# Performance work log

Measured on AMD Instinct MI355X. Metric: run time of the kernel, lower is better.

## Reference

```python
import jax, jax.numpy as jnp
import numpy as np

V, D, HID, HEADS = 50000, 128, 128, 4
N, E, G = 100000, 1600000, 256
CH = HID // HEADS  # per-head channels for layer 1


def setup_inputs() -> dict:
    key = jax.random.key(0)
    ks = jax.random.split(key, 16)
    g = lambda i, shape, scale=0.05: jax.random.normal(ks[i], shape, jnp.float32) * scale
    return {
        "x_lex": jax.random.randint(ks[0], (N,), 0, V),
        "edge_index": jax.random.randint(ks[1], (2, E), 0, N),
        "batch": jnp.sort(jax.random.randint(ks[2], (N,), 0, G)),
        "emb": g(3, (V, D)),
        "W1": g(4, (D, HID)), "a1_src": g(5, (HEADS, CH)), "a1_dst": g(6, (HEADS, CH)), "b1": jnp.zeros((HID,), jnp.float32),
        "W2": g(7, (HID, HID)), "a2_src": g(8, (1, HID)), "a2_dst": g(9, (1, HID)), "b2": jnp.zeros((HID,), jnp.float32),
        "Wc1": g(10, (HID, HID // 2)), "bc1": jnp.zeros((HID // 2,), jnp.float32),
        "Wc2": g(11, (HID // 2, 1)), "bc2": jnp.zeros((1,), jnp.float32),
    }


def gat_layer(x, src, dst, W, a_src, a_dst, b, heads, ch):
    """PyG-style GATConv (v1), concat=True, negative_slope=0.2."""
    n = x.shape[0]
    h = (x @ W).reshape(n, heads, ch)                 # [N,H,C]
    al_s = (h * a_src).sum(-1)                        # [N,H]
    al_d = (h * a_dst).sum(-1)                        # [N,H]
    e = jax.nn.leaky_relu(al_s[src] + al_d[dst], 0.2) # [Etot,H]
    # segment softmax over incoming edges per destination node
    m = jax.ops.segment_max(e, dst, num_segments=n)
    ex = jnp.exp(e - m[dst])
    s = jax.ops.segment_sum(ex, dst, num_segments=n)
    alpha = ex / s[dst]
    out = jax.ops.segment_sum(alpha[:, :, None] * h[src], dst, num_segments=n)  # [N,H,C]
    return out.reshape(n, heads * ch) + b


def reference(x_lex, edge_index, batch, emb, W1, a1_src, a1_dst, b1, W2, a2_src, a2_dst, b2, Wc1, bc1, Wc2, bc2):
    n = x_lex.shape[0]
    loops = jnp.arange(n)  # GATConv adds self-loops by default
    src = jnp.concatenate([edge_index[0], loops])
    dst = jnp.concatenate([edge_index[1], loops])
    x = emb[x_lex]                                               # [N,D]
    h = jax.nn.elu(gat_layer(x, src, dst, W1, a1_src, a1_dst, b1, HEADS, CH))
    h = jax.nn.elu(gat_layer(h, src, dst, W2, a2_src, a2_dst, b2, 1, HID))
    sums = jax.ops.segment_sum(h, batch, num_segments=G)
    cnt = jax.ops.segment_sum(jnp.ones((n,), h.dtype), batch, num_segments=G)
    h_pool = sums / jnp.maximum(cnt, 1.0)[:, None]               # global mean pool [G,HID]
    logits = jax.nn.relu(h_pool @ Wc1 + bc1) @ Wc2 + bc2         # [G,1]
    return (logits, h_pool)
```

## Files before the change

kernel.cpp:

```cpp
#include <hip/hip_runtime.h>
#include <hip/hip_bf16.h>
#include <math.h>

#define P_CHUNK 8192
#define NBKT 1024

__device__ __forceinline__ float lrelu(float x){ return x < 0.f ? 0.2f*x : x; }
__device__ __forceinline__ float elu_(float x){ return x > 0.f ? x : expm1f(x); }

__global__ __launch_bounds__(256) void p1hist(const int* __restrict__ ei, int E, int Etot,
                                              int* __restrict__ totals){
  __shared__ int lh[NBKT];
  int tid = threadIdx.x;
  for (int t = tid; t < NBKT; t += 256) lh[t] = 0;
  __syncthreads();
  int base = blockIdx.x * P_CHUNK;
  for (int j = 0; j < P_CHUNK; j += 256){
    int i = base + j + tid;
    if (i < Etot){
      int dst = (i < E) ? ei[E + i] : (i - E);
      atomicAdd(&lh[dst >> 7], 1);
    }
  }
  __syncthreads();
  for (int t = tid; t < NBKT; t += 256){
    int v = lh[t];
    if (v) atomicAdd(&totals[t], v);
  }
}

__global__ __launch_bounds__(256) void p2scan(const int* __restrict__ totals,
                                              int* __restrict__ bbase, int* __restrict__ bcur,
                                              int Etot, int* __restrict__ off, int N){
  __shared__ int wsum[4];
  __shared__ int runsh;
  int tid = threadIdx.x, lane = tid & 63, w = tid >> 6;
  if (tid == 0) runsh = 0;
  __syncthreads();
  for (int c = 0; c < NBKT; c += 256){
    int v = totals[c + tid];
    int x = v;
    #pragma unroll
    for (int d = 1; d < 64; d <<= 1){ int y = __shfl_up(x, d); if (lane >= d) x += y; }
    if (lane == 63) wsum[w] = x;
    __syncthreads();
    int wpre = 0;
    for (int i = 0; i < w; i++) wpre += wsum[i];
    int run = runsh;
    int excl = run + wpre + x - v;
    bbase[c + tid] = excl;
    bcur[c + tid]  = excl;
    __syncthreads();
    if (tid == 0) runsh = run + wsum[0] + wsum[1] + wsum[2] + wsum[3];
    __syncthreads();
  }
  if (tid == 0){ bbase[NBKT] = Etot; off[N] = Etot; }
}

__global__ __launch_bounds__(256) void p3scatter(const int* __restrict__ ei, int E, int Etot,
                                                 int* __restrict__ bcur, int2* __restrict__ tmp){
  __shared__ int lh[NBKT];
  __shared__ int lbase[NBKT];
  int tid = threadIdx.x;
  for (int t = tid; t < NBKT; t += 256) lh[t] = 0;
  __syncthreads();
  int base = blockIdx.x * P_CHUNK;
  for (int j = 0; j < P_CHUNK; j += 256){
    int i = base + j + tid;
    if (i < Etot){
      int dst = (i < E) ? ei[E + i] : (i - E);
      atomicAdd(&lh[dst >> 7], 1);
    }
  }
  __syncthreads();
  for (int t = tid; t < NBKT; t += 256){
    int v = lh[t];
    lbase[t] = v ? atomicAdd(&bcur[t], v) : 0;
  }
  __syncthreads();
  for (int t = tid; t < NBKT; t += 256) lh[t] = 0;
  __syncthreads();
  for (int j = 0; j < P_CHUNK; j += 256){
    int i = base + j + tid;
    if (i < Etot){
      int s, d;
      if (i < E){ s = ei[i]; d = ei[E + i]; } else { s = i - E; d = i - E; }
      int b = d >> 7;
      int r = atomicAdd(&lh[b], 1);
      tmp[lbase[b] + r] = make_int2(s, d);
    }
  }
}

__global__ __launch_bounds__(256) void p4local(const int2* __restrict__ tmp,
                                               const int* __restrict__ bbase,
                                               int* __restrict__ off, int* __restrict__ srcs, int N){
  __shared__ int cnt[128];
  __shared__ int offL[128];
  int b = blockIdx.x, tid = threadIdx.x;
  int e0 = bbase[b], e1 = bbase[b + 1];
  if (tid < 128) cnt[tid] = 0;
  __syncthreads();
  for (int j = e0 + tid; j < e1; j += 256)
    atomicAdd(&cnt[tmp[j].y & 127], 1);
  __syncthreads();
  if (tid < 64){
    int v0 = cnt[2*tid], v1 = cnt[2*tid + 1];
    int p = v0 + v1;
    int x = p;
    #pragma unroll
    for (int d = 1; d < 64; d <<= 1){ int y = __shfl_up(x, d); if (tid >= d) x += y; }
    int excl = x - p;
    offL[2*tid]     = excl;
    offL[2*tid + 1] = excl + v0;
  }
  __syncthreads();
  if (tid < 128){
    int gd = b*128 + tid;
    if (gd < N) off[gd] = e0 + offL[tid];
    cnt[tid] = 0;
  }
  __syncthreads();
  for (int j = e0 + tid; j < e1; j += 256){
    int2 e = tmp[j];
    int d = e.y & 127;
    int r = atomicAdd(&cnt[d], 1);
    srcs[e0 + offL[d] + r] = e.x;
  }
}

template<int H, bool GATHER>
__global__ __launch_bounds__(256) void gemm_al(
    const float* __restrict__ X, const int* __restrict__ idx,
    const float* __restrict__ W, const float* __restrict__ asrc,
    const float* __restrict__ adst, float* __restrict__ Hout,
    float* __restrict__ als, float* __restrict__ ald, int n)
{
  __shared__ float xs[128][68];
  __shared__ float wch[32][128];
  int tid = threadIdx.x;
  int tr = tid >> 5, tc = tid & 31;
  int r8 = tr*8, c4 = tc*4;
  int row0 = blockIdx.x * 64;

  #pragma unroll
  for (int j=0;j<8;j++){
    int e = tid + j*256;
    int r = e >> 5, cq = e & 31;
    int gr = row0 + r;
    float4 v = make_float4(0.f,0.f,0.f,0.f);
    if (gr < n){
      int srow = GATHER ? idx[gr] : gr;
      v = *reinterpret_cast<const float4*>(&X[(size_t)srow*128 + cq*4]);
    }
    xs[cq*4+0][r] = v.x;
    xs[cq*4+1][r] = v.y;
    xs[cq*4+2][r] = v.z;
    xs[cq*4+3][r] = v.w;
  }

  float acc[8][4];
  #pragma unroll
  for (int r=0;r<8;r++)
    #pragma unroll
    for (int i=0;i<4;i++) acc[r][i] = 0.f;

  for (int kc=0;kc<4;kc++){
    __syncthreads();
    #pragma unroll
    for (int j=0;j<4;j++){
      int e = tid + j*256;
      int r = e>>5, cq = e&31;
      *reinterpret_cast<float4*>(&wch[r][cq*4]) =
        *reinterpret_cast<const float4*>(&W[(size_t)(kc*32+r)*128 + cq*4]);
    }
    __syncthreads();
    #pragma unroll
    for (int kk=0;kk<32;kk++){
      int k = kc*32+kk;
      const float4 x0 = *reinterpret_cast<const float4*>(&xs[k][r8]);
      const float4 x1 = *reinterpret_cast<const float4*>(&xs[k][r8+4]);
      const float4 wv = *reinterpret_cast<const float4*>(&wch[kk][c4]);
      acc[0][0]=fmaf(x0.x,wv.x,acc[0][0]); acc[0][1]=fmaf(x0.x,wv.y,acc[0][1]);
      acc[0][2]=fmaf(x0.x,wv.z,acc[0][2]); acc[0][3]=fmaf(x0.x,wv.w,acc[0][3]);
      acc[1][0]=fmaf(x0.y,wv.x,acc[1][0]); acc[1][1]=fmaf(x0.y,wv.y,acc[1][1]);
      acc[1][2]=fmaf(x0.y,wv.z,acc[1][2]); acc[1][3]=fmaf(x0.y,wv.w,acc[1][3]);
      acc[2][0]=fmaf(x0.z,wv.x,acc[2][0]); acc[2][1]=fmaf(x0.z,wv.y,acc[2][1]);
      acc[2][2]=fmaf(x0.z,wv.z,acc[2][2]); acc[2][3]=fmaf(x0.z,wv.w,acc[2][3]);
      acc[3][0]=fmaf(x0.w,wv.x,acc[3][0]); acc[3][1]=fmaf(x0.w,wv.y,acc[3][1]);
      acc[3][2]=fmaf(x0.w,wv.z,acc[3][2]); acc[3][3]=fmaf(x0.w,wv.w,acc[3][3]);
      acc[4][0]=fmaf(x1.x,wv.x,acc[4][0]); acc[4][1]=fmaf(x1.x,wv.y,acc[4][1]);
      acc[4][2]=fmaf(x1.x,wv.z,acc[4][2]); acc[4][3]=fmaf(x1.x,wv.w,acc[4][3]);
      acc[5][0]=fmaf(x1.y,wv.x,acc[5][0]); acc[5][1]=fmaf(x1.y,wv.y,acc[5][1]);
      acc[5][2]=fmaf(x1.y,wv.z,acc[5][2]); acc[5][3]=fmaf(x1.y,wv.w,acc[5][3]);
      acc[6][0]=fmaf(x1.z,wv.x,acc[6][0]); acc[6][1]=fmaf(x1.z,wv.y,acc[6][1]);
      acc[6][2]=fmaf(x1.z,wv.z,acc[6][2]); acc[6][3]=fmaf(x1.z,wv.w,acc[6][3]);
      acc[7][0]=fmaf(x1.w,wv.x,acc[7][0]); acc[7][1]=fmaf(x1.w,wv.y,acc[7][1]);
      acc[7][2]=fmaf(x1.w,wv.z,acc[7][2]); acc[7][3]=fmaf(x1.w,wv.w,acc[7][3]);
    }
  }

  const float4 asv = *reinterpret_cast<const float4*>(&asrc[c4]);
  const float4 adv = *reinterpret_cast<const float4*>(&adst[c4]);
  const int GT = 32 / H;
  int hh = tc / GT;

  #pragma unroll
  for (int r=0;r<8;r++){
    int gr = row0 + r8 + r;
    if (gr < n){
      *reinterpret_cast<float4*>(&Hout[(size_t)gr*128 + c4]) =
        make_float4(acc[r][0], acc[r][1], acc[r][2], acc[r][3]);
    }
    float ps = acc[r][0]*asv.x + acc[r][1]*asv.y + acc[r][2]*asv.z + acc[r][3]*asv.w;
    float pd = acc[r][0]*adv.x + acc[r][1]*adv.y + acc[r][2]*adv.z + acc[r][3]*adv.w;
    #pragma unroll
    for (int m=1;m<GT;m<<=1){ ps += __shfl_xor(ps,m); pd += __shfl_xor(pd,m); }
    if ((tc & (GT-1)) == 0 && gr < n){
      als[(size_t)gr*H + hh] = ps;
      ald[(size_t)gr*H + hh] = pd;
    }
  }
}

template<int H>
__global__ __launch_bounds__(256) void aggr(
    const float* __restrict__ h, const float* __restrict__ als,
    const float* __restrict__ ald, const int* __restrict__ srcs,
    const int* __restrict__ off, const float* __restrict__ bias,
    float* __restrict__ out, int n)
{
  __shared__ float s_p[4][64*H];
  __shared__ int   s_s[4][64];
  int tid = threadIdx.x;
  int wid = tid >> 6, lane = tid & 63;
  int d = blockIdx.x*4 + wid;
  if (d >= n) return;
  int half = lane >> 5, ch = lane & 31;
  int c4 = ch*4;
  const int hh = (H==1) ? 0 : (ch >> 3);

  int s0 = off[d], s1 = off[d+1];

  float adv[H];
  #pragma unroll
  for (int q=0;q<H;q++) adv[q] = ald[(size_t)d*H + q];

  float m[H], ssum[H];
  #pragma unroll
  for (int q=0;q<H;q++){ m[q] = -INFINITY; ssum[q] = 0.f; }
  float a0=0.f, a1=0.f, a2=0.f, a3=0.f;

  for (int base = s0; base < s1; base += 64){
    int cl = s1 - base; if (cl > 64) cl = 64;

    int sv = 0;
    float e[H];
    if (lane < cl){
      sv = srcs[base + lane];
      #pragma unroll
      for (int q=0;q<H;q++) e[q] = lrelu(als[(size_t)sv*H + q] + adv[q]);
    } else {
      #pragma unroll
      for (int q=0;q<H;q++) e[q] = -INFINITY;
    }

    float cm[H];
    #pragma unroll
    for (int q=0;q<H;q++) cm[q] = e[q];
    #pragma unroll
    for (int sh=1; sh<64; sh<<=1){
      #pragma unroll
      for (int q=0;q<H;q++) cm[q] = fmaxf(cm[q], __shfl_xor(cm[q], sh));
    }

    float p[H], sc[H];
    #pragma unroll
    for (int q=0;q<H;q++){
      float nm = fmaxf(m[q], cm[q]);
      sc[q] = __expf(m[q] - nm);
      ssum[q] *= sc[q];
      m[q] = nm;
      p[q] = __expf(e[q] - nm);
    }
    float schh = sc[0];
    #pragma unroll
    for (int q=1;q<H;q++) schh = (hh==q) ? sc[q] : schh;
    a0 *= schh; a1 *= schh; a2 *= schh; a3 *= schh;

    float cs[H];
    #pragma unroll
    for (int q=0;q<H;q++) cs[q] = p[q];
    #pragma unroll
    for (int sh=1; sh<64; sh<<=1){
      #pragma unroll
      for (int q=0;q<H;q++) cs[q] += __shfl_xor(cs[q], sh);
    }
    #pragma unroll
    for (int q=0;q<H;q++) ssum[q] += cs[q];

    #pragma unroll
    for (int q=0;q<H;q++) s_p[wid][lane*H + q] = p[q];
    s_s[wid][lane] = sv;

    for (int j = half; j < cl; j += 2){
      int s = s_s[wid][j];
      float w = s_p[wid][j*H + hh];
      const float4 hv = *reinterpret_cast<const float4*>(&h[(size_t)s*128 + c4]);
      a0 = fmaf(w, hv.x, a0);
      a1 = fmaf(w, hv.y, a1);
      a2 = fmaf(w, hv.z, a2);
      a3 = fmaf(w, hv.w, a3);
    }
  }

  a0 += __shfl_xor(a0, 32);
  a1 += __shfl_xor(a1, 32);
  a2 += __shfl_xor(a2, 32);
  a3 += __shfl_xor(a3, 32);

  float den = ssum[0];
  #pragma unroll
  for (int q=1;q<H;q++) den = (hh==q) ? ssum[q] : den;
  float inv = 1.f / den;

  if (half == 0){
    const float4 bv = *reinterpret_cast<const float4*>(&bias[c4]);
    float4 o;
    o.x = elu_(a0*inv + bv.x);
    o.y = elu_(a1*inv + bv.y);
    o.z = elu_(a2*inv + bv.z);
    o.w = elu_(a3*inv + bv.w);
    *reinterpret_cast<float4*>(&out[(size_t)d*128 + c4]) = o;
  }
}

__global__ __launch_bounds__(256) void kpool(const float* __restrict__ act,
    const int* __restrict__ batch, int n, float* __restrict__ pool)
{
  __shared__ int sb[2];
  __shared__ float part[128];
  int g = blockIdx.x, tid = threadIdx.x;
  if (tid == 0){
    int lo=0, hi=n;
    while (lo<hi){ int mid=(lo+hi)>>1; if (batch[mid] < g) lo=mid+1; else hi=mid; }
    sb[0]=lo;
    int lo2=lo, hi2=n;
    while (lo2<hi2){ int mid=(lo2+hi2)>>1; if (batch[mid] < g+1) lo2=mid+1; else hi2=mid; }
    sb[1]=lo2;
  }
  __syncthreads();
  int lo=sb[0], hi=sb[1];
  int c = tid & 127, half = tid >> 7;
  float acc = 0.f;
  for (int i=lo+half; i<hi; i+=2) acc += act[(size_t)i*128 + c];
  if (half == 0) part[c] = acc;
  __syncthreads();
  if (half == 1) part[c] += acc;
  __syncthreads();
  if (half == 0){
    float cnt = (float)(hi-lo);
    pool[(size_t)g*128 + c] = part[c] / fmaxf(cnt, 1.f);
  }
}

__global__ __launch_bounds__(64) void kclassify(const float* __restrict__ pool,
    const float* __restrict__ Wc1, const float* __restrict__ bc1,
    const float* __restrict__ Wc2, const float* __restrict__ bc2,
    float* __restrict__ logits)
{
  int g = blockIdx.x, j = threadIdx.x;
  const float* hp = pool + (size_t)g*128;
  float t = bc1[j];
  #pragma unroll 8
  for (int c=0;c<128;c++) t = fmaf(hp[c], Wc1[c*64+j], t);
  t = fmaxf(t, 0.f) * Wc2[j];
  for (int m=1;m<64;m<<=1) t += __shfl_xor(t, m);
  if (j==0) logits[g] = t + bc2[0];
}

extern "C" void kernel_launch(void* const* d_in, const int* in_sizes, int n_in,
                              void* d_out, int out_size, void* d_ws, size_t ws_size,
                              hipStream_t stream)
{
  const int*   x_lex = (const int*)d_in[0];
  const int*   ei    = (const int*)d_in[1];
  const int*   batch = (const int*)d_in[2];
  const float* emb   = (const float*)d_in[3];
  const float* W1    = (const float*)d_in[4];
  const float* a1s   = (const float*)d_in[5];
  const float* a1d   = (const float*)d_in[6];
  const float* b1    = (const float*)d_in[7];
  const float* W2    = (const float*)d_in[8];
  const float* a2s   = (const float*)d_in[9];
  const float* a2d   = (const float*)d_in[10];
  const float* b2    = (const float*)d_in[11];
  const float* Wc1   = (const float*)d_in[12];
  const float* bc1   = (const float*)d_in[13];
  const float* Wc2   = (const float*)d_in[14];
  const float* bc2   = (const float*)d_in[15];

  int N = in_sizes[0];
  int E = in_sizes[1] / 2;
  int Etot = E + N;
  const int G = 256;

  char* p = (char*)d_ws;
  float* hbuf   = (float*)p;          p += (size_t)N*128*4;
  float* act    = (float*)p;          p += (size_t)N*128*4;
  float* als    = (float*)p;          p += (size_t)N*4*4;
  float* ald    = (float*)p;          p += (size_t)N*4*4;
  int*   off    = (int*)p;            p += (size_t)(N+1)*4;
  int*   srcs   = (int*)p;            p += (size_t)Etot*4;
  int*   totals = (int*)p;            p += NBKT*4;
  int*   bbase  = (int*)p;            p += (NBKT+1)*4;
  int*   bcur   = (int*)p;
  int2*  tmp    = (int2*)hbuf;

  hipMemsetAsync(totals, 0, NBKT*4, stream);
  int nblk = (Etot + P_CHUNK - 1) / P_CHUNK;
  int nb   = (N + 127) / 128;
  p1hist   <<<nblk,256,0,stream>>>(ei, E, Etot, totals);
  p2scan   <<<1,   256,0,stream>>>(totals, bbase, bcur, Etot, off, N);
  p3scatter<<<nblk,256,0,stream>>>(ei, E, Etot, bcur, tmp);
  p4local  <<<nb,  256,0,stream>>>(tmp, bbase, off, srcs, N);

  int gb = (N + 63)/64;
  gemm_al<4,true ><<<gb,256,0,stream>>>(emb, x_lex, W1, a1s, a1d, hbuf, als, ald, N);
  aggr<4><<<(N+3)/4,256,0,stream>>>(hbuf, als, ald, srcs, off, b1, act, N);

  gemm_al<1,false><<<gb,256,0,stream>>>(act, nullptr, W2, a2s, a2d, hbuf, als, ald, N);
  aggr<1><<<(N+3)/4,256,0,stream>>>(hbuf, als, ald, srcs, off, b2, act, N);

  float* out = (float*)d_out;
  kpool<<<G,256,0,stream>>>(act, batch, N, out + G);
  kclassify<<<G,64,0,stream>>>(out + G, Wc1, bc1, Wc2, bc2, out);
}
```

Baseline: 528.3 us.

## Pack edge temp to 32-bit, row-major GEMM tile, nontemporal aggr stores

Packs the temporary (src, local dst) edge pair into a single 32-bit int (17 bits of source, 7 bits of local destination), halving the scatter and local-sort traffic. Changes the GEMM shared X tile from transposed to row-major with vector stores and a k-by-4 inner loop, removing the scalar transposing stores. Uses nontemporal stores for the aggregation output. The packing assumes N fits in 17 bits and is wrong for larger graphs.

```diff
diff --git a/kernel.cpp b/kernel.cpp
--- a/kernel.cpp
+++ b/kernel.cpp
@@ -4,6 +4,8 @@
 
 #define P_CHUNK 8192
 #define NBKT 1024
+
+typedef float f4 __attribute__((ext_vector_type(4)));
 
 __device__ __forceinline__ float lrelu(float x){ return x < 0.f ? 0.2f*x : x; }
 __device__ __forceinline__ float elu_(float x){ return x > 0.f ? x : expm1f(x); }
@@ -58,7 +60,7 @@
 }
 
 __global__ __launch_bounds__(256) void p3scatter(const int* __restrict__ ei, int E, int Etot,
-                                                 int* __restrict__ bcur, int2* __restrict__ tmp){
+                                                 int* __restrict__ bcur, int* __restrict__ tmp){
   __shared__ int lh[NBKT];
   __shared__ int lbase[NBKT];
   int tid = threadIdx.x;
@@ -87,12 +89,12 @@
       if (i < E){ s = ei[i]; d = ei[E + i]; } else { s = i - E; d = i - E; }
       int b = d >> 7;
       int r = atomicAdd(&lh[b], 1);
-      tmp[lbase[b] + r] = make_int2(s, d);
-    }
-  }
-}
-
-__global__ __launch_bounds__(256) void p4local(const int2* __restrict__ tmp,
+      tmp[lbase[b] + r] = s | ((d & 127) << 17);
+    }
+  }
+}
+
+__global__ __launch_bounds__(256) void p4local(const int* __restrict__ tmp,
                                                const int* __restrict__ bbase,
                                                int* __restrict__ off, int* __restrict__ srcs, int N){
   __shared__ int cnt[128];
@@ -102,7 +104,7 @@
   if (tid < 128) cnt[tid] = 0;
   __syncthreads();
   for (int j = e0 + tid; j < e1; j += 256)
-    atomicAdd(&cnt[tmp[j].y & 127], 1);
+    atomicAdd(&cnt[(tmp[j] >> 17) & 127], 1);
   __syncthreads();
   if (tid < 64){
     int v0 = cnt[2*tid], v1 = cnt[2*tid + 1];
@@ -122,10 +124,10 @@
   }
   __syncthreads();
   for (int j = e0 + tid; j < e1; j += 256){
-    int2 e = tmp[j];
-    int d = e.y & 127;
+    int e = tmp[j];
+    int d = (e >> 17) & 127;
     int r = atomicAdd(&cnt[d], 1);
-    srcs[e0 + offL[d] + r] = e.x;
+    srcs[e0 + offL[d] + r] = e & 0x1FFFF;
   }
 }
 
@@ -136,7 +138,7 @@
     const float* __restrict__ adst, float* __restrict__ Hout,
     float* __restrict__ als, float* __restrict__ ald, int n)
 {
-  __shared__ float xs[128][68];
+  __shared__ float xs[64][132];
   __shared__ float wch[32][128];
   int tid = threadIdx.x;
   int tr = tid >> 5, tc = tid & 31;
@@ -148,15 +150,12 @@
     int e = tid + j*256;
     int r = e >> 5, cq = e & 31;
     int gr = row0 + r;
-    float4 v = make_float4(0.f,0.f,0.f,0.f);
+    f4 v = (f4)(0.f);
     if (gr < n){
       int srow = GATHER ? idx[gr] : gr;
-      v = *reinterpret_cast<const float4*>(&X[(size_t)srow*128 + cq*4]);
-    }
-    xs[cq*4+0][r] = v.x;
-    xs[cq*4+1][r] = v.y;
-    xs[cq*4+2][r] = v.z;
-    xs[cq*4+3][r] = v.w;
+      v = *reinterpret_cast<const f4*>(&X[(size_t)srow*128 + cq*4]);
+    }
+    *reinterpret_cast<f4*>(&xs[r][cq*4]) = v;
   }
 
   float acc[8][4];
@@ -171,37 +170,30 @@
     for (int j=0;j<4;j++){
       int e = tid + j*256;
       int r = e>>5, cq = e&31;
-      *reinterpret_cast<float4*>(&wch[r][cq*4]) =
-        *reinterpret_cast<const float4*>(&W[(size_t)(kc*32+r)*128 + cq*4]);
+      *reinterpret_cast<f4*>(&wch[r][cq*4]) =
+        *reinterpret_cast<const f4*>(&W[(size_t)(kc*32+r)*128 + cq*4]);
     }
     __syncthreads();
     #pragma unroll
-    for (int kk=0;kk<32;kk++){
-      int k = kc*32+kk;
-      const float4 x0 = *reinterpret_cast<const float4*>(&xs[k][r8]);
-      const float4 x1 = *reinterpret_cast<const float4*>(&xs[k][r8+4]);
-      const float4 wv = *reinterpret_cast<const float4*>(&wch[kk][c4]);
-      acc[0][0]=fmaf(x0.x,wv.x,acc[0][0]); acc[0][1]=fmaf(x0.x,wv.y,acc[0][1]);
-      acc[0][2]=fmaf(x0.x,wv.z,acc[0][2]); acc[0][3]=fmaf(x0.x,wv.w,acc[0][3]);
-      acc[1][0]=fmaf(x0.y,wv.x,acc[1][0]); acc[1][1]=fmaf(x0.y,wv.y,acc[1][1]);
-      acc[1][2]=fmaf(x0.y,wv.z,acc[1][2]); acc[1][3]=fmaf(x0.y,wv.w,acc[1][3]);
-      acc[2][0]=fmaf(x0.z,wv.x,acc[2][0]); acc[2][1]=fmaf(x0.z,wv.y,acc[2][1]);
-      acc[2][2]=fmaf(x0.z,wv.z,acc[2][2]); acc[2][3]=fmaf(x0.z,wv.w,acc[2][3]);
-      acc[3][0]=fmaf(x0.w,wv.x,acc[3][0]); acc[3][1]=fmaf(x0.w,wv.y,acc[3][1]);
-      acc[3][2]=fmaf(x0.w,wv.z,acc[3][2]); acc[3][3]=fmaf(x0.w,wv.w,acc[3][3]);
-      acc[4][0]=fmaf(x1.x,wv.x,acc[4][0]); acc[4][1]=fmaf(x1.x,wv.y,acc[4][1]);
-      acc[4][2]=fmaf(x1.x,wv.z,acc[4][2]); acc[4][3]=fmaf(x1.x,wv.w,acc[4][3]);
-      acc[5][0]=fmaf(x1.y,wv.x,acc[5][0]); acc[5][1]=fmaf(x1.y,wv.y,acc[5][1]);
-      acc[5][2]=fmaf(x1.y,wv.z,acc[5][2]); acc[5][3]=fmaf(x1.y,wv.w,acc[5][3]);
-      acc[6][0]=fmaf(x1.z,wv.x,acc[6][0]); acc[6][1]=fmaf(x1.z,wv.y,acc[6][1]);
-      acc[6][2]=fmaf(x1.z,wv.z,acc[6][2]); acc[6][3]=fmaf(x1.z,wv.w,acc[6][3]);
-      acc[7][0]=fmaf(x1.w,wv.x,acc[7][0]); acc[7][1]=fmaf(x1.w,wv.y,acc[7][1]);
-      acc[7][2]=fmaf(x1.w,wv.z,acc[7][2]); acc[7][3]=fmaf(x1.w,wv.w,acc[7][3]);
-    }
-  }
-
-  const float4 asv = *reinterpret_cast<const float4*>(&asrc[c4]);
-  const float4 adv = *reinterpret_cast<const float4*>(&adst[c4]);
+    for (int kq=0;kq<8;kq++){
+      int k0 = kc*32 + kq*4;
+      f4 xv[8], wv[4];
+      #pragma unroll
+      for (int i=0;i<8;i++) xv[i] = *reinterpret_cast<const f4*>(&xs[r8+i][k0]);
+      #pragma unroll
+      for (int kk=0;kk<4;kk++) wv[kk] = *reinterpret_cast<const f4*>(&wch[kq*4+kk][c4]);
+      #pragma unroll
+      for (int kk=0;kk<4;kk++)
+        #pragma unroll
+        for (int i=0;i<8;i++)
+          #pragma unroll
+          for (int j=0;j<4;j++)
+            acc[i][j] = fmaf(xv[i][kk], wv[kk][j], acc[i][j]);
+    }
+  }
+
+  const f4 asv = *reinterpret_cast<const f4*>(&asrc[c4]);
+  const f4 adv = *reinterpret_cast<const f4*>(&adst[c4]);
   const int GT = 32 / H;
   int hh = tc / GT;
 
@@ -209,11 +201,11 @@
   for (int r=0;r<8;r++){
     int gr = row0 + r8 + r;
     if (gr < n){
-      *reinterpret_cast<float4*>(&Hout[(size_t)gr*128 + c4]) =
-        make_float4(acc[r][0], acc[r][1], acc[r][2], acc[r][3]);
-    }
-    float ps = acc[r][0]*asv.x + acc[r][1]*asv.y + acc[r][2]*asv.z + acc[r][3]*asv.w;
-    float pd = acc[r][0]*adv.x + acc[r][1]*adv.y + acc[r][2]*adv.z + acc[r][3]*adv.w;
+      f4 o = { acc[r][0], acc[r][1], acc[r][2], acc[r][3] };
+      *reinterpret_cast<f4*>(&Hout[(size_t)gr*128 + c4]) = o;
+    }
+    float ps = acc[r][0]*asv[0] + acc[r][1]*asv[1] + acc[r][2]*asv[2] + acc[r][3]*asv[3];
+    float pd = acc[r][0]*adv[0] + acc[r][1]*adv[1] + acc[r][2]*adv[2] + acc[r][3]*adv[3];
     #pragma unroll
     for (int m=1;m<GT;m<<=1){ ps += __shfl_xor(ps,m); pd += __shfl_xor(pd,m); }
     if ((tc & (GT-1)) == 0 && gr < n){
@@ -325,13 +317,13 @@
   float inv = 1.f / den;
 
   if (half == 0){
-    const float4 bv = *reinterpret_cast<const float4*>(&bias[c4]);
-    float4 o;
-    o.x = elu_(a0*inv + bv.x);
-    o.y = elu_(a1*inv + bv.y);
-    o.z = elu_(a2*inv + bv.z);
-    o.w = elu_(a3*inv + bv.w);
-    *reinterpret_cast<float4*>(&out[(size_t)d*128 + c4]) = o;
+    const f4 bv = *reinterpret_cast<const f4*>(&bias[c4]);
+    f4 o;
+    o[0] = elu_(a0*inv + bv[0]);
+    o[1] = elu_(a1*inv + bv[1]);
+    o[2] = elu_(a2*inv + bv[2]);
+    o[3] = elu_(a3*inv + bv[3]);
+    __builtin_nontemporal_store(o, reinterpret_cast<f4*>(&out[(size_t)d*128 + c4]));
   }
 }
 
@@ -415,7 +407,7 @@
   int*   totals = (int*)p;            p += NBKT*4;
   int*   bbase  = (int*)p;            p += (NBKT+1)*4;
   int*   bcur   = (int*)p;
-  int2*  tmp    = (int2*)hbuf;
+  int*   tmp    = (int*)hbuf;
 
   hipMemsetAsync(totals, 0, NBKT*4, stream);
   int nblk = (Etot + P_CHUNK - 1) / P_CHUNK;
```

Result: slower. 556.9 us (+5.4%).
